# Kernel optimization log

Measured on AMD Instinct MI355X. Metric: run time of the kernel, lower is better.

## Reference

```python
import jax, jax.numpy as jnp
import numpy as np

N = 8192          # points
M = 3             # point dimension
K_ORDER = 4       # tensor order k
C = 64            # input_in_channel
KNN = 16          # n_neighbors
NEG_SLOPE = 0.2
EPS = 1e-6


def vn_leaky_relu(v, U, neg_slope=NEG_SLOPE, eps=EPS):
    """Vector-neuron LeakyReLU. v: (n, T, C), U: (C, C) learned direction map."""
    d = jnp.einsum('ntc,cd->ntd', v, U)
    dot = jnp.sum(v * d, axis=1, keepdims=True)        # (n,1,C)
    dn2 = jnp.sum(d * d, axis=1, keepdims=True)        # (n,1,C)
    proj = (dot / (dn2 + eps)) * d
    return neg_slope * v + (1.0 - neg_slope) * jnp.where(dot >= 0, v, v - proj)


def contract_pairs(x, w, k):
    """Learned combination of all pairwise traces.
    x: (n, m,...,m (k axes), C); w: (k*(k-1)//2, C). Returns order k-2 tensor."""
    pairs = [(a, b) for a in range(1, k + 1) for b in range(a + 1, k + 1)]
    acc = None
    for i, (a, b) in enumerate(pairs):
        t = jnp.trace(x, axis1=a, axis2=b)             # (n, m^(k-2)..., C)
        acc = t * w[i] if acc is None else acc + t * w[i]
    return acc


def setup_inputs() -> dict:
    key = jax.random.key(0)
    ks = jax.random.split(key, 8)
    s1 = 1.0 / np.sqrt(C)
    s2 = 1.0 / np.sqrt(2 * C)
    return {
        'x': jax.random.normal(ks[0], (N, M), dtype=jnp.float32),
        'kron_W': jax.random.normal(ks[1], (K_ORDER, C, C), dtype=jnp.float32) * s1,
        'kron_U': jax.random.normal(ks[2], (K_ORDER, C, C), dtype=jnp.float32) * s1,
        'contr_w4': jax.random.normal(ks[3], (6, 2 * C), dtype=jnp.float32) * s2,
        'contr_W': jax.random.normal(ks[4], (2 * C, 2 * C), dtype=jnp.float32) * s2,
        'contr_U': jax.random.normal(ks[5], (2 * C, 2 * C), dtype=jnp.float32) * s2,
        'contr_w2': jax.random.normal(ks[6], (1, 2 * C), dtype=jnp.float32) * s2,
    }


def reference(x, kron_W, kron_U, contr_w4, contr_W, contr_U, contr_w2):
    n, m = x.shape
    c = kron_W.shape[-1]
    # --- brute-force kNN on x (replaces sklearn fit/kneighbors; self included,
    # static because dynamic_knn=False) ---
    sq = jnp.sum(x * x, axis=1)
    d2 = sq[:, None] + sq[None, :] - 2.0 * (x @ x.T)   # (n,n)
    _, idx = jax.lax.top_k(-d2, KNN)                   # (n,KNN) neighbor indices
    xg = x[idx]                                        # (n,KNN,m) gathered coords
    # --- Kronecker stage: v_{t+1}[i] = mean_{j in N(i)} x_j (x) v_t[j] ---
    v = jnp.ones((n, 1, c), dtype=x.dtype)
    for t in range(kron_W.shape[0]):
        vg = v[idx]                                    # (n,KNN,m^t,c)
        v = jnp.einsum('nka,nkbc->nabc', xg, vg) / KNN # (n,m,m^t,c)
        v = v.reshape(n, -1, c)                        # (n,m^(t+1),c)
        v = v @ kron_W[t]                              # CustomLinear (no bias)
        v = vn_leaky_relu(v, kron_U[t])
    # --- mean pooling + concat (pool_type=mean) ---
    g = jnp.mean(v, axis=0, keepdims=True)
    v = jnp.concatenate([v, jnp.broadcast_to(g, v.shape)], axis=2)  # (n,m^k,2c)
    c2 = 2 * c
    k = kron_W.shape[0]
    h = v.reshape((n,) + (m,) * k + (c2,))             # (n,3,3,3,3,2c)
    # --- contraction stage: k=4 -> 2 -> 0 ---
    h = contract_pairs(h, contr_w4, k)                 # (n,m,m,2c)
    h = h.reshape(n, m * m, c2) @ contr_W              # CustomLinear
    h = vn_leaky_relu(h, contr_U)
    h = h.reshape(n, m, m, c2)
    out = contract_pairs(h, contr_w2, 2)               # (n,2c)
    return out
```

## Files before the change

### kernel.cpp

```cpp
#include <hip/hip_runtime.h>
#include <math.h>

#define NPTS 8192
#define KNB  16
#define C1   64
#define C2   128
#define NEG  0.2f
#define VEPS 1e-6f
#define NCH  32
#define CHSZ (NPTS/NCH)

__device__ __forceinline__ unsigned long long expand10(unsigned v) {
    unsigned long long r = v & 0x3FFu;
    r = (r | (r << 16)) & 0x030000FFULL;
    r = (r | (r <<  8)) & 0x0300F00FULL;
    r = (r | (r <<  4)) & 0x030C30C3ULL;
    r = (r | (r <<  2)) & 0x09249249ULL;
    return r;
}

__global__ __launch_bounds__(256) void keys_kernel(const float* __restrict__ x,
                                                   unsigned long long* __restrict__ keys)
{
    const int i = blockIdx.x * 256 + threadIdx.x;
    auto cell = [](float v) -> unsigned {
        float t = (v + 6.f) * (1024.f / 12.f);
        int c = (int)t;
        c = c < 0 ? 0 : (c > 1023 ? 1023 : c);
        return (unsigned)c;
    };
    const unsigned long long m = expand10(cell(x[3*i+0]))
                               | (expand10(cell(x[3*i+1])) << 1)
                               | (expand10(cell(x[3*i+2])) << 2);
    keys[i] = (m << 13) | (unsigned long long)i;
}

__global__ __launch_bounds__(256) void rank_zero(int* __restrict__ rk)
{
    rk[blockIdx.x * 256 + threadIdx.x] = 0;
}

__global__ __launch_bounds__(256) void rank_part(const unsigned long long* __restrict__ keys,
                                                 int* __restrict__ rk)
{
    __shared__ unsigned long long sk[1024];
    const int slice = blockIdx.x & 7;
    const int qg    = blockIdx.x >> 3;
    for (int j = threadIdx.x; j < 1024; j += 256) sk[j] = keys[slice*1024 + j];
    __syncthreads();
    const int i = qg*256 + threadIdx.x;
    const unsigned long long mine = keys[i];
    int r = 0;
    for (int j = 0; j < 1024; j += 4)
        r += (int)(sk[j] < mine) + (int)(sk[j+1] < mine)
           + (int)(sk[j+2] < mine) + (int)(sk[j+3] < mine);
    atomicAdd(&rk[i], r);
}

__global__ __launch_bounds__(256) void rank_scatter(const int* __restrict__ rk,
                                                    const float* __restrict__ x,
                                                    float* __restrict__ xp,
                                                    int* __restrict__ perm)
{
    const int i = blockIdx.x * 256 + threadIdx.x;
    const int r = rk[i];
    perm[r] = i;
    xp[3*r+0] = x[3*i+0]; xp[3*r+1] = x[3*i+1]; xp[3*r+2] = x[3*i+2];
}

__global__ __launch_bounds__(256) void knn_part(const float* __restrict__ x,
                                                unsigned long long* __restrict__ parts)
{
    __shared__ __align__(16) float4 cpt[CHSZ];
    __shared__ unsigned long long sbuf[256 * 9];

    const int tid   = threadIdx.x;
    const int chunk = blockIdx.x & (NCH - 1);
    const int qg    = blockIdx.x >> 5;
    const int j0    = chunk * CHSZ;

    cpt[tid] = make_float4(x[3*(j0+tid)+0], x[3*(j0+tid)+1], x[3*(j0+tid)+2], 0.f);
    const int q = qg * 256 + tid;
    const float qx = x[3*q+0], qy = x[3*q+1], qz = x[3*q+2];

    float thrF;
    {
        int lo = q - 7; lo = lo < 0 ? 0 : (lo > NPTS-16 ? NPTS-16 : lo);
        float mx = 0.f;
#pragma unroll
        for (int s = 0; s < 16; ++s) {
            const float dx = qx - x[3*(lo+s)+0];
            const float dy = qy - x[3*(lo+s)+1];
            const float dz = qz - x[3*(lo+s)+2];
            mx = fmaxf(mx, fmaf(dx, dx, fmaf(dy, dy, dz*dz)));
        }
        thrF = mx * 1.0002f;
    }
    __syncthreads();

    unsigned long long bd[16];
#pragma unroll
    for (int r = 0; r < 16; ++r) bd[r] = ~0ull;
    int cnt = 0;
    unsigned long long* mybuf = sbuf + tid * 9;

    auto flush = [&]() {
#pragma unroll
        for (int s = 0; s < 8; ++s) {
            if (s < cnt) {
                const unsigned long long k = mybuf[s];
                if (k < bd[15]) {
#pragma unroll
                    for (int p2 = 15; p2 > 0; --p2) {
                        const bool sh = k < bd[p2-1];
                        const bool pl = k < bd[p2];
                        bd[p2] = sh ? bd[p2-1] : (pl ? k : bd[p2]);
                    }
                    if (k < bd[0]) bd[0] = k;
                }
            }
        }
        cnt = 0;
        if (bd[15] != ~0ull) {
            const double dub = __longlong_as_double((long long)(bd[15] | 8191ull));
            thrF = fminf(thrF, (float)dub * 1.0001f);
        }
    };

    for (int jj = 0; jj < CHSZ; jj += 4) {
        const float4 p0 = cpt[jj+0];
        const float4 p1 = cpt[jj+1];
        const float4 p2 = cpt[jj+2];
        const float4 p3 = cpt[jj+3];
#pragma unroll
        for (int u = 0; u < 4; ++u) {
            const float4 p = (u==0) ? p0 : (u==1) ? p1 : (u==2) ? p2 : p3;
            const float dx = qx - p.x, dy = qy - p.y, dz = qz - p.z;
            const float d2f = fmaf(dx, dx, fmaf(dy, dy, dz*dz));
            if (d2f <= thrF) {
                const double ddx = (double)dx, ddy = (double)dy, ddz = (double)dz;
                const double d2 = ddx*ddx + ddy*ddy + ddz*ddz;
                const unsigned long long key =
                    (((unsigned long long)__double_as_longlong(d2)) & ~8191ull)
                    | (unsigned long long)(j0 + jj + u);
                if (key < bd[15]) { mybuf[cnt] = key; ++cnt; }
            }
        }
        if (__any(cnt >= 5)) flush();
    }
    flush();

#pragma unroll
    for (int r = 0; r < 16; ++r)
        parts[((size_t)chunk * KNB + r) * NPTS + q] = bd[r];
}

__global__ __launch_bounds__(256) void knn_merge(const unsigned long long* __restrict__ parts,
                                                 int* __restrict__ idx_out)
{
    __shared__ unsigned char heads[256][NCH];
    const int tid = threadIdx.x;
    const int q = blockIdx.x * 256 + tid;
    unsigned char* h = heads[tid];
#pragma unroll
    for (int c = 0; c < NCH; ++c) h[c] = 0;
    for (int r = 0; r < KNB; ++r) {
        unsigned long long best = ~0ull; int bc = 0;
#pragma unroll
        for (int c = 0; c < NCH; ++c) {
            const unsigned long long k = parts[((size_t)c * KNB + h[c]) * NPTS + q];
            if (k < best) { best = k; bc = c; }
        }
        h[bc]++;
        idx_out[q*KNB + r] = (int)(best & 8191ull);
    }
}

__global__ __launch_bounds__(256) void prep_kernel(const float* __restrict__ kW,
                                                   const float* __restrict__ kU,
                                                   float* __restrict__ scol,
                                                   float* __restrict__ bcat)
{
    __shared__ float sW[64*64];
    __shared__ float sS[64];
    const int t = blockIdx.x;
    const int tid = threadIdx.x;
    if (t == 0) {
        for (int e = tid; e < 64*64; e += 256) sW[e] = kW[e];
        __syncthreads();
        if (tid < 64) {
            float s = 0.f;
            for (int j = 0; j < 64; ++j) s += sW[j*64 + tid];
            sS[tid] = s;
        }
        __syncthreads();
        if (tid < 64) {
            float s2 = 0.f;
            for (int j = 0; j < 64; ++j) s2 = fmaf(sS[j], kU[j*64 + tid], s2);
            scol[tid]      = sS[tid];
            scol[64 + tid] = s2;
        }
    } else {
        const float* W = kW + t*4096;
        const float* U = kU + t*4096;
        for (int e = tid; e < 64*64; e += 256) sW[e] = W[e];
        __syncthreads();
        float* B = bcat + (size_t)(t-1)*64*128;
        for (int o = tid; o < 64*64; o += 256) {
            const int j = o >> 6, c = o & 63;
            float s = 0.f;
            for (int l = 0; l < 64; ++l) s = fmaf(sW[j*64 + l], U[l*64 + c], s);
            B[j*128 + c]      = sW[j*64 + c];
            B[j*128 + 64 + c] = s;
        }
    }
}

__global__ __launch_bounds__(256) void step1_kernel(const float* __restrict__ xp,
                                                    const int* __restrict__ idxs,
                                                    const float* __restrict__ scol,
                                                    float* __restrict__ R1)
{
    const int pt = blockIdx.x * 256 + threadIdx.x;
    float mx0 = 0.f, mx1 = 0.f, mx2 = 0.f;
#pragma unroll
    for (int k = 0; k < KNB; ++k) {
        const int id = idxs[pt*KNB + k];
        mx0 += xp[3*id+0]; mx1 += xp[3*id+1]; mx2 += xp[3*id+2];
    }
    const float inv = 1.0f / KNB;
    mx0 *= inv; mx1 *= inv; mx2 *= inv;
    const float S2 = mx0*mx0 + mx1*mx1 + mx2*mx2;
    float* op = R1 + (size_t)pt * 192;
    for (int c = 0; c < 64; ++c) {
        const float sc = scol[c], su = scol[64 + c];
        const float dt = S2 * sc * su;
        const float dn = S2 * su * su;
        const float m  = (dt < 0.f) ? 0.8f * dt / (dn + VEPS) : 0.f;
        const float rc = fmaf(-m, su, sc);
        op[c]       = mx0 * rc;
        op[64 + c]  = mx1 * rc;
        op[128 + c] = mx2 * rc;
    }
}

#define FMA4(ar, b0, b1, b2, b3, acc) \
    acc.x = fmaf(ar.x,b0.x, fmaf(ar.y,b1.x, fmaf(ar.z,b2.x, fmaf(ar.w,b3.x, acc.x)))); \
    acc.y = fmaf(ar.x,b0.y, fmaf(ar.y,b1.y, fmaf(ar.z,b2.y, fmaf(ar.w,b3.y, acc.y)))); \
    acc.z = fmaf(ar.x,b0.z, fmaf(ar.y,b1.z, fmaf(ar.z,b2.z, fmaf(ar.w,b3.z, acc.z)))); \
    acc.w = fmaf(ar.x,b0.w, fmaf(ar.y,b1.w, fmaf(ar.z,b2.w, fmaf(ar.w,b3.w, acc.w))));

__global__ __launch_bounds__(256) void zgemm_kernel(const float* __restrict__ R,
                                                    const float* __restrict__ Bcat,
                                                    float* __restrict__ YwZ)
{
    constexpr int SA = 68;
    __shared__ __align__(16) float sA[64*SA];
    __shared__ __align__(16) float sB[64*128];
    const int tid = threadIdx.x;
    const size_t row0 = (size_t)blockIdx.x * 64;

    for (int e4 = tid; e4 < 1024; e4 += 256) {
        const int r = e4 >> 4, c4 = (e4 & 15) * 4;
        *reinterpret_cast<float4*>(sA + r*SA + c4) =
            *reinterpret_cast<const float4*>(R + (row0 + r)*64 + c4);
    }
    for (int e4 = tid; e4 < 2048; e4 += 256) {
        const int j = e4 >> 5, c4 = (e4 & 31) * 4;
        *reinterpret_cast<float4*>(sB + j*128 + c4) =
            *reinterpret_cast<const float4*>(Bcat + j*128 + c4);
    }
    __syncthreads();

    const int rg = tid >> 5;
    const int d  = (tid & 31) * 4;
    float4 acc0={0,0,0,0},acc1=acc0,acc2=acc0,acc3=acc0,acc4=acc0,acc5=acc0,acc6=acc0,acc7=acc0;
    for (int c = 0; c < 64; c += 4) {
        const float4 b0 = *reinterpret_cast<const float4*>(sB + (c+0)*128 + d);
        const float4 b1 = *reinterpret_cast<const float4*>(sB + (c+1)*128 + d);
        const float4 b2 = *reinterpret_cast<const float4*>(sB + (c+2)*128 + d);
        const float4 b3 = *reinterpret_cast<const float4*>(sB + (c+3)*128 + d);
        float4 a;
        a = *reinterpret_cast<const float4*>(sA + (rg*8+0)*SA + c); FMA4(a,b0,b1,b2,b3,acc0);
        a = *reinterpret_cast<const float4*>(sA + (rg*8+1)*SA + c); FMA4(a,b0,b1,b2,b3,acc1);
        a = *reinterpret_cast<const float4*>(sA + (rg*8+2)*SA + c); FMA4(a,b0,b1,b2,b3,acc2);
        a = *reinterpret_cast<const float4*>(sA + (rg*8+3)*SA + c); FMA4(a,b0,b1,b2,b3,acc3);
        a = *reinterpret_cast<const float4*>(sA + (rg*8+4)*SA + c); FMA4(a,b0,b1,b2,b3,acc4);
        a = *reinterpret_cast<const float4*>(sA + (rg*8+5)*SA + c); FMA4(a,b0,b1,b2,b3,acc5);
        a = *reinterpret_cast<const float4*>(sA + (rg*8+6)*SA + c); FMA4(a,b0,b1,b2,b3,acc6);
        a = *reinterpret_cast<const float4*>(sA + (rg*8+7)*SA + c); FMA4(a,b0,b1,b2,b3,acc7);
    }
    float* op = YwZ + (row0 + rg*8)*128 + d;
    *reinterpret_cast<float4*>(op + 0*128) = acc0;
    *reinterpret_cast<float4*>(op + 1*128) = acc1;
    *reinterpret_cast<float4*>(op + 2*128) = acc2;
    *reinterpret_cast<float4*>(op + 3*128) = acc3;
    *reinterpret_cast<float4*>(op + 4*128) = acc4;
    *reinterpret_cast<float4*>(op + 5*128) = acc5;
    *reinterpret_cast<float4*>(op + 6*128) = acc6;
    *reinterpret_cast<float4*>(op + 7*128) = acc7;
}

template<int PINP, int TT>
__global__ __launch_bounds__(256) void gather_kernel(
    const float* __restrict__ xp, const int* __restrict__ idxs,
    const float* __restrict__ yz,
    float* __restrict__ Rout,
    int ppb)
{
    constexpr int PCW = PINP * 128;
    constexpr int NSL = PCW / 4;
    constexpr int TC  = TT * 64;

    __shared__ __align__(16) float buf[TT * 128];
    __shared__ int   sIds[KNB];
    __shared__ float sXg[KNB*3];
    __shared__ float pdt[4][64], pdn[4][64], msc[64];

    const int tid   = threadIdx.x;
    const int slots = gridDim.x >> 3;
    const int xcd   = blockIdx.x & 7;
    const int slot  = blockIdx.x >> 3;
    const int base  = xcd * slots * ppb;

    for (int pi = 0; pi < ppb; ++pi) {
        const int pt = base + pi * slots + slot;
        if (tid < KNB) {
            const int id = idxs[pt*KNB + tid];
            sIds[tid] = id;
            sXg[tid*3+0] = xp[3*id+0];
            sXg[tid*3+1] = xp[3*id+1];
            sXg[tid*3+2] = xp[3*id+2];
        }
        __syncthreads();

        float xr[KNB*3];
#pragma unroll
        for (int e = 0; e < KNB*3; ++e) xr[e] = sXg[e];

        for (int sl = tid; sl < NSL; sl += 256) {
            const int b  = sl >> 5;
            const int cc = (sl & 31) * 4;
            float4 s0 = {0,0,0,0}, s1 = s0, s2 = s0;
#pragma unroll
            for (int k = 0; k < KNB; ++k) {
                const float4 val = *reinterpret_cast<const float4*>(
                    yz + (size_t)sIds[k]*PCW + b*128 + cc);
                const float xa = xr[k*3+0], xb = xr[k*3+1], xc = xr[k*3+2];
                s0.x=fmaf(xa,val.x,s0.x); s0.y=fmaf(xa,val.y,s0.y);
                s0.z=fmaf(xa,val.z,s0.z); s0.w=fmaf(xa,val.w,s0.w);
                s1.x=fmaf(xb,val.x,s1.x); s1.y=fmaf(xb,val.y,s1.y);
                s1.z=fmaf(xb,val.z,s1.z); s1.w=fmaf(xb,val.w,s1.w);
                s2.x=fmaf(xc,val.x,s2.x); s2.y=fmaf(xc,val.y,s2.y);
                s2.z=fmaf(xc,val.z,s2.z); s2.w=fmaf(xc,val.w,s2.w);
            }
            const float inv = 1.0f / KNB;
            s0.x*=inv; s0.y*=inv; s0.z*=inv; s0.w*=inv;
            s1.x*=inv; s1.y*=inv; s1.z*=inv; s1.w*=inv;
            s2.x*=inv; s2.y*=inv; s2.z*=inv; s2.w*=inv;
            *reinterpret_cast<float4*>(buf + (0*PINP + b)*128 + cc) = s0;
            *reinterpret_cast<float4*>(buf + (1*PINP + b)*128 + cc) = s1;
            *reinterpret_cast<float4*>(buf + (2*PINP + b)*128 + cc) = s2;
        }
        __syncthreads();
        {
            const int c = tid & 63, g = tid >> 6;
            float dt = 0.f, dn = 0.f;
            for (int t = g; t < TT; t += 4) {
                const float vv = buf[t*128 + c], dd = buf[t*128 + 64 + c];
                dt = fmaf(vv, dd, dt); dn = fmaf(dd, dd, dn);
            }
            pdt[g][c] = dt; pdn[g][c] = dn;
        }
        __syncthreads();
        if (tid < 64) {
            const float dt = pdt[0][tid]+pdt[1][tid]+pdt[2][tid]+pdt[3][tid];
            const float dn = pdn[0][tid]+pdn[1][tid]+pdn[2][tid]+pdn[3][tid];
            msc[tid] = (dt < 0.f) ? 0.8f * dt / (dn + VEPS) : 0.f;
        }
        __syncthreads();
        {
            float* op = Rout + (size_t)pt * TC;
            for (int e = tid; e < TC; e += 256) {
                const int t = e >> 6, c = e & 63;
                op[e] = fmaf(-msc[c], buf[t*128 + 64 + c], buf[t*128 + c]);
            }
        }
        __syncthreads();
    }
}

#define FMAQS(acc, s, val) \
    acc.x = fmaf(s, val.x, acc.x); acc.y = fmaf(s, val.y, acc.y); \
    acc.z = fmaf(s, val.z, acc.z); acc.w = fmaf(s, val.w, acc.w);

__global__ __launch_bounds__(256) void gather4_kernel(
    const float* __restrict__ xp, const int* __restrict__ idxs,
    const float* __restrict__ yz,
    const float* __restrict__ w4,
    float* __restrict__ hv, float* __restrict__ gpart,
    int ppb)
{
    constexpr int TT = 81;
    constexpr int CH = 32;
    constexpr int SB = 68;
    constexpr int NG = (TT*CH + 255) / 256;

    __shared__ __align__(16) float buf[TT * SB];
    __shared__ int   sIds[KNB];
    __shared__ float sXg[KNB*3];
    __shared__ float pdt[27][33], pdn[27][33];
    __shared__ float msc[CH];

    const int tid   = threadIdx.x;
    const int xcd   = blockIdx.x & 7;
    const int r2    = blockIdx.x >> 3;
    const int half  = r2 & 1;
    const int slot  = r2 >> 1;
    const int slots = gridDim.x >> 4;
    const int base0 = xcd * slots * ppb;
    const int c0    = half * CH;
    const int eff   = xcd * slots + slot;

    const int ub  = tid >> 3;
    const int ucq = tid & 7;
    const bool act = (ub < 27);
    const int srcV = ub*128 + c0 + ucq*4;
    const int srcD = srcV + 64;

    float gacc[NG];
#pragma unroll
    for (int i = 0; i < NG; ++i) gacc[i] = 0.f;

    for (int pi = 0; pi < ppb; ++pi) {
        const int pt = base0 + pi * slots + slot;
        if (tid < KNB) {
            const int id = idxs[pt*KNB + tid];
            sIds[tid] = id;
            sXg[tid*3+0] = xp[3*id+0];
            sXg[tid*3+1] = xp[3*id+1];
            sXg[tid*3+2] = xp[3*id+2];
        }
        __syncthreads();

        if (act) {
            float4 vA[3], dA[3];
#pragma unroll
            for (int a = 0; a < 3; ++a) { vA[a] = make_float4(0,0,0,0); dA[a] = vA[a]; }
#pragma unroll
            for (int k = 0; k < KNB; ++k) {
                const float* rowp = yz + (size_t)sIds[k]*3456;
                const float4 vq = *reinterpret_cast<const float4*>(rowp + srcV);
                const float4 dq = *reinterpret_cast<const float4*>(rowp + srcD);
                const float xa = sXg[k*3+0], xb = sXg[k*3+1], xc = sXg[k*3+2];
                FMAQS(vA[0], xa, vq) FMAQS(vA[1], xb, vq) FMAQS(vA[2], xc, vq)
                FMAQS(dA[0], xa, dq) FMAQS(dA[1], xb, dq) FMAQS(dA[2], xc, dq)
            }
            const float inv = 1.0f / KNB;
            float4 dt4 = make_float4(0,0,0,0), dn4 = dt4;
#pragma unroll
            for (int a = 0; a < 3; ++a) {
                vA[a].x*=inv; vA[a].y*=inv; vA[a].z*=inv; vA[a].w*=inv;
                dA[a].x*=inv; dA[a].y*=inv; dA[a].z*=inv; dA[a].w*=inv;
                dt4.x = fmaf(vA[a].x, dA[a].x, dt4.x);
                dt4.y = fmaf(vA[a].y, dA[a].y, dt4.y);
                dt4.z = fmaf(vA[a].z, dA[a].z, dt4.z);
                dt4.w = fmaf(vA[a].w, dA[a].w, dt4.w);
                dn4.x = fmaf(dA[a].x, dA[a].x, dn4.x);
                dn4.y = fmaf(dA[a].y, dA[a].y, dn4.y);
                dn4.z = fmaf(dA[a].z, dA[a].z, dn4.z);
                dn4.w = fmaf(dA[a].w, dA[a].w, dn4.w);
                float* bp = buf + (a*27 + ub)*SB;
                *reinterpret_cast<float4*>(bp + ucq*4)      = vA[a];
                *reinterpret_cast<float4*>(bp + 32 + ucq*4) = dA[a];
            }
            pdt[ub][ucq*4+0] = dt4.x; pdt[ub][ucq*4+1] = dt4.y;
            pdt[ub][ucq*4+2] = dt4.z; pdt[ub][ucq*4+3] = dt4.w;
            pdn[ub][ucq*4+0] = dn4.x; pdn[ub][ucq*4+1] = dn4.y;
            pdn[ub][ucq*4+2] = dn4.z; pdn[ub][ucq*4+3] = dn4.w;
        }
        __syncthreads();
        if (tid < CH) {
            float dt = 0.f, dn = 0.f;
#pragma unroll
            for (int b2 = 0; b2 < 27; ++b2) { dt += pdt[b2][tid]; dn += pdn[b2][tid]; }
            msc[tid] = (dt < 0.f) ? 0.8f * dt / (dn + VEPS) : 0.f;
        }
        __syncthreads();
#pragma unroll
        for (int i = 0; i < NG; ++i) {
            const int e = i*256 + tid;
            if (e < TT*CH) {
                const int t = e >> 5, cc = e & 31;
                const float v = fmaf(-msc[cc], buf[t*SB + 32 + cc], buf[t*SB + cc]);
                buf[t*SB + cc] = v;
                gacc[i] += v;
            }
        }
        __syncthreads();
        for (int e = tid; e < 9*CH; e += 256) {
            const int pq = e >> 5, cc = e & 31;
            const int p = pq / 3, qq = pq - 3*p;
            const int c = c0 + cc;
            float tr0=0,tr1=0,tr2=0,tr3=0,tr4=0,tr5=0;
#pragma unroll
            for (int r = 0; r < 3; ++r) {
                tr0 += buf[(r*36 + p*3 + qq )*SB + cc];
                tr1 += buf[(r*30 + p*9 + qq )*SB + cc];
                tr2 += buf[(r*28 + p*9 + qq*3)*SB + cc];
                tr3 += buf[(p*27 + r*12 + qq )*SB + cc];
                tr4 += buf[(p*27 + r*10 + qq*3)*SB + cc];
                tr5 += buf[(p*27 + qq*9 + r*4 )*SB + cc];
            }
            hv[(size_t)pt*576 + pq*64 + c] =
                  w4[0*C2 + c]*tr0 + w4[1*C2 + c]*tr1 + w4[2*C2 + c]*tr2
                + w4[3*C2 + c]*tr3 + w4[4*C2 + c]*tr4 + w4[5*C2 + c]*tr5;
        }
        __syncthreads();
    }
    float* gp = gpart + (size_t)eff * 5184;
#pragma unroll
    for (int i = 0; i < NG; ++i) {
        const int e = i*256 + tid;
        if (e < TT*CH) {
            const int t = e >> 5, cc = e & 31;
            gp[t*64 + c0 + cc] = gacc[i];
        }
    }
}

__global__ __launch_bounds__(256) void reduce_g_kernel(const float* __restrict__ gpart,
                                                       float* __restrict__ g)
{
    __shared__ float red[256];
    const int el = threadIdx.x & 15, pg = threadIdx.x >> 4;
    const int e = blockIdx.x * 16 + el;
    float s = 0.f;
    for (int p = pg; p < 2048; p += 16) s += gpart[(size_t)p * (81*C1) + e];
    red[threadIdx.x] = s;
    __syncthreads();
    for (int st = 8; st > 0; st >>= 1) {
        if (pg < st) red[el + 16*pg] += red[el + 16*(pg+st)];
        __syncthreads();
    }
    if (pg == 0) g[e] = red[el] * (1.0f/NPTS);
}

__global__ __launch_bounds__(256) void hgw_kernel(const float* __restrict__ g,
                                                  const float* __restrict__ w4,
                                                  const float* __restrict__ cW,
                                                  float* __restrict__ hgW)
{
    __shared__ float gs[81*C1];
    __shared__ float hg[9*C1];
    const int tid = threadIdx.x;
    for (int e = tid; e < 81*C1; e += 256) gs[e] = g[e];
    __syncthreads();
    for (int e = tid; e < 9*C1; e += 256) {
        const int pq = e >> 6, c = e & 63;
        const int p = pq / 3, qq = pq - 3*p;
        float tr0=0,tr1=0,tr2=0,tr3=0,tr4=0,tr5=0;
#pragma unroll
        for (int r = 0; r < 3; ++r) {
            tr0 += gs[(r*36 + p*3 + qq ) * C1 + c];
            tr1 += gs[(r*30 + p*9 + qq ) * C1 + c];
            tr2 += gs[(r*28 + p*9 + qq*3) * C1 + c];
            tr3 += gs[(p*27 + r*12 + qq ) * C1 + c];
            tr4 += gs[(p*27 + r*10 + qq*3) * C1 + c];
            tr5 += gs[(p*27 + qq*9 + r*4 ) * C1 + c];
        }
        hg[e] = w4[0*C2 + 64 + c]*tr0 + w4[1*C2 + 64 + c]*tr1 + w4[2*C2 + 64 + c]*tr2
              + w4[3*C2 + 64 + c]*tr3 + w4[4*C2 + 64 + c]*tr4 + w4[5*C2 + 64 + c]*tr5;
    }
    __syncthreads();
    for (int o = tid; o < 9*C2; o += 256) {
        const int t = o >> 7, c = o & 127;
        float s = 0.f;
        for (int j = 0; j < C1; ++j) s = fmaf(hg[t*C1 + j], cW[(C1+j)*C2 + c], s);
        hgW[o] = s;
    }
}

__global__ __launch_bounds__(256) void contract_kernel(const float* __restrict__ hv,
                                                       const float* __restrict__ hgW,
                                                       const float* __restrict__ cW,
                                                       const float* __restrict__ cU,
                                                       const float* __restrict__ w2,
                                                       const int* __restrict__ perm,
                                                       float* __restrict__ out,
                                                       int ppb)
{
    constexpr int S0 = C1 + 4;
    constexpr int SH = C2 + 4;
    __shared__ __align__(16) float h0[36*S0];
    __shared__ __align__(16) float h1[36*SH];
    __shared__ __align__(16) float h2[36*SH];
    __shared__ __align__(16) float hgs[9*C2];
    __shared__ int sPerm[4];

    const int tid = threadIdx.x;
    for (int e = tid; e < 9*C2; e += 256) hgs[e] = hgW[e];
    __syncthreads();

    const int iters = ppb >> 2;
    for (int it = 0; it < iters; ++it) {
        const int base = blockIdx.x * ppb + it * 4;
        if (tid < 4) sPerm[tid] = perm[base + tid];
        for (int e = tid; e < 4*9*C1; e += 256) {
            const int pt = e / 576, rem = e - pt*576;
            const int t = rem >> 6, c = rem & 63;
            h0[(pt*9 + t)*S0 + c] = hv[(size_t)(base+pt)*576 + rem];
        }
        __syncthreads();
        for (int u = tid; u < 9*32; u += 256) {
            const int tg = u >> 5;
            const int d  = (u & 31) * 4;
            const int r0 = tg*4;
            float4 acc0 = *reinterpret_cast<const float4*>(hgs + ((r0+0)%9)*C2 + d);
            float4 acc1 = *reinterpret_cast<const float4*>(hgs + ((r0+1)%9)*C2 + d);
            float4 acc2 = *reinterpret_cast<const float4*>(hgs + ((r0+2)%9)*C2 + d);
            float4 acc3 = *reinterpret_cast<const float4*>(hgs + ((r0+3)%9)*C2 + d);
            for (int c = 0; c < C1; c += 4) {
                const float4 a0 = *reinterpret_cast<const float4*>(h0 + (r0+0)*S0 + c);
                const float4 a1 = *reinterpret_cast<const float4*>(h0 + (r0+1)*S0 + c);
                const float4 a2 = *reinterpret_cast<const float4*>(h0 + (r0+2)*S0 + c);
                const float4 a3 = *reinterpret_cast<const float4*>(h0 + (r0+3)*S0 + c);
                const float4 b0 = *reinterpret_cast<const float4*>(cW + (c+0)*C2 + d);
                const float4 b1 = *reinterpret_cast<const float4*>(cW + (c+1)*C2 + d);
                const float4 b2 = *reinterpret_cast<const float4*>(cW + (c+2)*C2 + d);
                const float4 b3 = *reinterpret_cast<const float4*>(cW + (c+3)*C2 + d);
                FMA4(a0, b0, b1, b2, b3, acc0);
                FMA4(a1, b0, b1, b2, b3, acc1);
                FMA4(a2, b0, b1, b2, b3, acc2);
                FMA4(a3, b0, b1, b2, b3, acc3);
            }
            *reinterpret_cast<float4*>(h1 + (r0+0)*SH + d) = acc0;
            *reinterpret_cast<float4*>(h1 + (r0+1)*SH + d) = acc1;
            *reinterpret_cast<float4*>(h1 + (r0+2)*SH + d) = acc2;
            *reinterpret_cast<float4*>(h1 + (r0+3)*SH + d) = acc3;
        }
        __syncthreads();
        for (int u = tid; u < 9*32; u += 256) {
            const int tg = u >> 5;
            const int d  = (u & 31) * 4;
            const int r0 = tg*4;
            float4 acc0 = {0,0,0,0}, acc1 = acc0, acc2 = acc0, acc3 = acc0;
            for (int c = 0; c < C2; c += 4) {
                const float4 a0 = *reinterpret_cast<const float4*>(h1 + (r0+0)*SH + c);
                const float4 a1 = *reinterpret_cast<const float4*>(h1 + (r0+1)*SH + c);
                const float4 a2 = *reinterpret_cast<const float4*>(h1 + (r0+2)*SH + c);
                const float4 a3 = *reinterpret_cast<const float4*>(h1 + (r0+3)*SH + c);
                const float4 b0 = *reinterpret_cast<const float4*>(cU + (c+0)*C2 + d);
                const float4 b1 = *reinterpret_cast<const float4*>(cU + (c+1)*C2 + d);
                const float4 b2 = *reinterpret_cast<const float4*>(cU + (c+2)*C2 + d);
                const float4 b3 = *reinterpret_cast<const float4*>(cU + (c+3)*C2 + d);
                FMA4(a0, b0, b1, b2, b3, acc0);
                FMA4(a1, b0, b1, b2, b3, acc1);
                FMA4(a2, b0, b1, b2, b3, acc2);
                FMA4(a3, b0, b1, b2, b3, acc3);
            }
            *reinterpret_cast<float4*>(h2 + (r0+0)*SH + d) = acc0;
            *reinterpret_cast<float4*>(h2 + (r0+1)*SH + d) = acc1;
            *reinterpret_cast<float4*>(h2 + (r0+2)*SH + d) = acc2;
            *reinterpret_cast<float4*>(h2 + (r0+3)*SH + d) = acc3;
        }
        __syncthreads();
#pragma unroll
        for (int p2 = 0; p2 < 2; ++p2) {
            const int pair = tid + 256*p2;
            const int pt = pair >> 7, c = pair & 127;
            float dt = 0.f, dn = 0.f;
            for (int t = 0; t < 9; ++t) {
                const float vv = h1[(pt*9+t)*SH + c], dd = h2[(pt*9+t)*SH + c];
                dt = fmaf(vv, dd, dt); dn = fmaf(dd, dd, dn);
            }
            const float m = (dt < 0.f) ? 0.8f * dt / (dn + VEPS) : 0.f;
            float s = 0.f;
#pragma unroll
            for (int r = 0; r < 3; ++r) {
                const int t = r * 4;
                s += fmaf(-m, h2[(pt*9+t)*SH + c], h1[(pt*9+t)*SH + c]);
            }
            out[(size_t)sPerm[pt]*C2 + c] = w2[c] * s;
        }
        __syncthreads();
    }
}

extern "C" void kernel_launch(void* const* d_in, const int* in_sizes, int n_in,
                              void* d_out, int out_size, void* d_ws, size_t ws_size,
                              hipStream_t stream)
{
    (void)in_sizes; (void)n_in; (void)out_size; (void)ws_size;
    const float* x  = (const float*)d_in[0];
    const float* kW = (const float*)d_in[1];
    const float* kU = (const float*)d_in[2];
    const float* w4 = (const float*)d_in[3];
    const float* cW = (const float*)d_in[4];
    const float* cU = (const float*)d_in[5];
    const float* w2 = (const float*)d_in[6];
    float* out = (float*)d_out;

    char* ws = (char*)d_ws;
    size_t off = 0;
    auto alloc = [&](size_t bytes) -> void* {
        void* p = ws + off; off += (bytes + 255) & ~(size_t)255; return p;
    };
    int*   idx   = (int*)  alloc((size_t)NPTS*KNB*4);
    float* xp    = (float*)alloc((size_t)NPTS*3*4);
    unsigned long long* keys = (unsigned long long*)alloc((size_t)NPTS*8);
    int*   perm  = (int*)  alloc((size_t)NPTS*4);
    int*   rk    = (int*)  alloc((size_t)NPTS*4);
    float* scol  = (float*)alloc(128*4);
    float* bcat  = (float*)alloc((size_t)3*64*128*4);
    float* R1    = (float*)alloc((size_t)NPTS*3*C1*4);
    float* YwZ2  = (float*)alloc((size_t)NPTS*3*C2*4);
    float* R2    = (float*)alloc((size_t)NPTS*9*C1*4);
    float* YwZ3  = (float*)alloc((size_t)NPTS*9*C2*4);
    float* R3    = (float*)alloc((size_t)NPTS*27*C1*4);
    float* YwZ4  = (float*)alloc((size_t)NPTS*27*C2*4);
    float* g     = (float*)alloc((size_t)81*C1*4);
    float* hgW   = (float*)alloc((size_t)9*C2*4);

    float* hv    = R1;
    float* gpart = R2;
    unsigned long long* parts = (unsigned long long*)YwZ4;

    keys_kernel <<<NPTS/256, 256, 0, stream>>>(x, keys);
    rank_zero   <<<NPTS/256, 256, 0, stream>>>(rk);
    rank_part   <<<256, 256, 0, stream>>>(keys, rk);
    rank_scatter<<<NPTS/256, 256, 0, stream>>>(rk, x, xp, perm);
    knn_part    <<<32*NCH, 256, 0, stream>>>(xp, parts);
    knn_merge   <<<NPTS/256, 256, 0, stream>>>(parts, idx);
    prep_kernel <<<4, 256, 0, stream>>>(kW, kU, scol, bcat);
    step1_kernel<<<NPTS/256, 256, 0, stream>>>(xp, idx, scol, R1);

    zgemm_kernel<<<NPTS*3/64,  256, 0, stream>>>(R1, bcat,            YwZ2);
    gather_kernel<3, 9>  <<<2048, 256, 0, stream>>>(xp, idx, YwZ2, R2, 4);
    zgemm_kernel<<<NPTS*9/64,  256, 0, stream>>>(R2, bcat + 8192,     YwZ3);
    gather_kernel<9, 27> <<<2048, 256, 0, stream>>>(xp, idx, YwZ3, R3, 4);
    zgemm_kernel<<<NPTS*27/64, 256, 0, stream>>>(R3, bcat + 16384,    YwZ4);
    gather4_kernel<<<4096, 256, 0, stream>>>(xp, idx, YwZ4, w4, hv, gpart, 4);

    reduce_g_kernel<<<324, 256, 0, stream>>>(gpart, g);
    hgw_kernel<<<1, 256, 0, stream>>>(g, w4, cW, hgW);
    contract_kernel<<<1024, 256, 0, stream>>>(hv, hgW, cW, cU, w2, perm, out, 8);
}
```

Baseline: 690.5 us.

## Cull kNN chunks per wavefront using chunk bounding boxes and precomputed seed thresholds

Precomputes each query's seed distance threshold in a separate kernel and each candidate chunk's axis-aligned bounding box in another. In knn_part, a wavefront whose queries all have a box lower bound above their threshold skips the chunk, writing sentinel keys instead of scanning 256 points. The block-wide shared load and barrier become per-wavefront private copies of the chunk, so waves can exit independently. This adds two small launches and four times the shared memory per block, which may lower occupancy.

Result: no change. 693.4 us (+0.4%).

```diff
diff --git a/kernel.cpp b/kernel.cpp
--- a/kernel.cpp
+++ b/kernel.cpp
@@ -68,35 +68,96 @@
     xp[3*r+0] = x[3*i+0]; xp[3*r+1] = x[3*i+1]; xp[3*r+2] = x[3*i+2];
 }
 
+__global__ __launch_bounds__(256) void seedthr_kernel(const float* __restrict__ xp,
+                                                      float* __restrict__ gthr)
+{
+    const int q = blockIdx.x * 256 + threadIdx.x;
+    const float qx = xp[3*q+0], qy = xp[3*q+1], qz = xp[3*q+2];
+    int lo = q - 7; lo = lo < 0 ? 0 : (lo > NPTS-16 ? NPTS-16 : lo);
+    float mx = 0.f;
+#pragma unroll
+    for (int s = 0; s < 16; ++s) {
+        const float dx = qx - xp[3*(lo+s)+0];
+        const float dy = qy - xp[3*(lo+s)+1];
+        const float dz = qz - xp[3*(lo+s)+2];
+        mx = fmaxf(mx, fmaf(dx, dx, fmaf(dy, dy, dz*dz)));
+    }
+    gthr[q] = mx * 1.0002f;
+}
+
+__global__ __launch_bounds__(256) void aabb_kernel(const float* __restrict__ xp,
+                                                   float* __restrict__ gaabb)
+{
+    __shared__ float wred[4][6];
+    const int chunk = blockIdx.x;
+    const int tid = threadIdx.x;
+    const int j = chunk * CHSZ + tid;
+    float mnx = xp[3*j+0], mny = xp[3*j+1], mnz = xp[3*j+2];
+    float mxx = mnx, mxy = mny, mxz = mnz;
+    for (int off = 32; off > 0; off >>= 1) {
+        mnx = fminf(mnx, __shfl_down(mnx, off));
+        mny = fminf(mny, __shfl_down(mny, off));
+        mnz = fminf(mnz, __shfl_down(mnz, off));
+        mxx = fmaxf(mxx, __shfl_down(mxx, off));
+        mxy = fmaxf(mxy, __shfl_down(mxy, off));
+        mxz = fmaxf(mxz, __shfl_down(mxz, off));
+    }
+    if ((tid & 63) == 0) {
+        const int w = tid >> 6;
+        wred[w][0]=mnx; wred[w][1]=mny; wred[w][2]=mnz;
+        wred[w][3]=mxx; wred[w][4]=mxy; wred[w][5]=mxz;
+    }
+    __syncthreads();
+    if (tid == 0) {
+        float a0=wred[0][0], a1=wred[0][1], a2=wred[0][2];
+        float a3=wred[0][3], a4=wred[0][4], a5=wred[0][5];
+        for (int w = 1; w < 4; ++w) {
+            a0=fminf(a0,wred[w][0]); a1=fminf(a1,wred[w][1]); a2=fminf(a2,wred[w][2]);
+            a3=fmaxf(a3,wred[w][3]); a4=fmaxf(a4,wred[w][4]); a5=fmaxf(a5,wred[w][5]);
+        }
+        gaabb[chunk*8+0]=a0; gaabb[chunk*8+1]=a1; gaabb[chunk*8+2]=a2;
+        gaabb[chunk*8+3]=a3; gaabb[chunk*8+4]=a4; gaabb[chunk*8+5]=a5;
+    }
+}
+
 __global__ __launch_bounds__(256) void knn_part(const float* __restrict__ x,
+                                                const float* __restrict__ gthr,
+                                                const float* __restrict__ gaabb,
                                                 unsigned long long* __restrict__ parts)
 {
-    __shared__ __align__(16) float4 cpt[CHSZ];
+    __shared__ __align__(16) float4 cpt[4 * CHSZ];
     __shared__ unsigned long long sbuf[256 * 9];
 
     const int tid   = threadIdx.x;
+    const int wv    = tid >> 6;
+    const int lane  = tid & 63;
     const int chunk = blockIdx.x & (NCH - 1);
     const int qg    = blockIdx.x >> 5;
     const int j0    = chunk * CHSZ;
-
-    cpt[tid] = make_float4(x[3*(j0+tid)+0], x[3*(j0+tid)+1], x[3*(j0+tid)+2], 0.f);
-    const int q = qg * 256 + tid;
+    const int q     = qg * 256 + tid;
+
     const float qx = x[3*q+0], qy = x[3*q+1], qz = x[3*q+2];
-
-    float thrF;
+    float thrF = gthr[q];
+
     {
-        int lo = q - 7; lo = lo < 0 ? 0 : (lo > NPTS-16 ? NPTS-16 : lo);
-        float mx = 0.f;
-#pragma unroll
-        for (int s = 0; s < 16; ++s) {
-            const float dx = qx - x[3*(lo+s)+0];
-            const float dy = qy - x[3*(lo+s)+1];
-            const float dz = qz - x[3*(lo+s)+2];
-            mx = fmaxf(mx, fmaf(dx, dx, fmaf(dy, dy, dz*dz)));
-        }
-        thrF = mx * 1.0002f;
-    }
-    __syncthreads();
+        const float dx = fmaxf(0.f, fmaxf(gaabb[chunk*8+0] - qx, qx - gaabb[chunk*8+3]));
+        const float dy = fmaxf(0.f, fmaxf(gaabb[chunk*8+1] - qy, qy - gaabb[chunk*8+4]));
+        const float dz = fmaxf(0.f, fmaxf(gaabb[chunk*8+2] - qz, qz - gaabb[chunk*8+5]));
+        const float lb = fmaf(dx, dx, fmaf(dy, dy, dz*dz)) * 0.9998f;
+        if (__all(lb > thrF)) {
+#pragma unroll
+            for (int r = 0; r < 16; ++r)
+                parts[((size_t)chunk * KNB + r) * NPTS + q] = ~0ull;
+            return;
+        }
+    }
+
+    float4* wcpt = cpt + wv * CHSZ;
+#pragma unroll
+    for (int s = 0; s < 4; ++s) {
+        const int j = lane + 64*s;
+        wcpt[j] = make_float4(x[3*(j0+j)+0], x[3*(j0+j)+1], x[3*(j0+j)+2], 0.f);
+    }
 
     unsigned long long bd[16];
 #pragma unroll
@@ -128,10 +189,10 @@
     };
 
     for (int jj = 0; jj < CHSZ; jj += 4) {
-        const float4 p0 = cpt[jj+0];
-        const float4 p1 = cpt[jj+1];
-        const float4 p2 = cpt[jj+2];
-        const float4 p3 = cpt[jj+3];
+        const float4 p0 = wcpt[jj+0];
+        const float4 p1 = wcpt[jj+1];
+        const float4 p2 = wcpt[jj+2];
+        const float4 p3 = wcpt[jj+3];
 #pragma unroll
         for (int u = 0; u < 4; ++u) {
             const float4 p = (u==0) ? p0 : (u==1) ? p1 : (u==2) ? p2 : p3;
@@ -711,6 +772,8 @@
     unsigned long long* keys = (unsigned long long*)alloc((size_t)NPTS*8);
     int*   perm  = (int*)  alloc((size_t)NPTS*4);
     int*   rk    = (int*)  alloc((size_t)NPTS*4);
+    float* gthr  = (float*)alloc((size_t)NPTS*4);
+    float* gaabb = (float*)alloc((size_t)NCH*8*4);
     float* scol  = (float*)alloc(128*4);
     float* bcat  = (float*)alloc((size_t)3*64*128*4);
     float* R1    = (float*)alloc((size_t)NPTS*3*C1*4);
@@ -730,7 +793,9 @@
     rank_zero   <<<NPTS/256, 256, 0, stream>>>(rk);
     rank_part   <<<256, 256, 0, stream>>>(keys, rk);
     rank_scatter<<<NPTS/256, 256, 0, stream>>>(rk, x, xp, perm);
-    knn_part    <<<32*NCH, 256, 0, stream>>>(xp, parts);
+    seedthr_kernel<<<NPTS/256, 256, 0, stream>>>(xp, gthr);
+    aabb_kernel <<<NCH, 256, 0, stream>>>(xp, gaabb);
+    knn_part    <<<32*NCH, 256, 0, stream>>>(xp, gthr, gaabb, parts);
     knn_merge   <<<NPTS/256, 256, 0, stream>>>(parts, idx);
     prep_kernel <<<4, 256, 0, stream>>>(kW, kU, scol, bcat);
     step1_kernel<<<NPTS/256, 256, 0, stream>>>(xp, idx, scol, R1);
```
